# Optimization experiments

Hardware: AMD Instinct MI355X
Metric: run time of the kernel (lower is better)

The kernel has to match this reference:

```python
import jax, jax.numpy as jnp
import numpy as np

D_MODEL, D_FF, N_EXPERTS, TOP_K = 1024, 4096, 8, 2


def setup_inputs() -> dict:
    key = jax.random.key(0)
    ks = jax.random.split(key, 7)
    s = 0.02
    return {
        "x": jax.random.normal(ks[0], (2, 2048, D_MODEL), dtype=jnp.float32),
        "router_w": jax.random.normal(ks[1], (D_MODEL, N_EXPERTS), dtype=jnp.float32) * s,
        "router_b": jnp.zeros((N_EXPERTS,), dtype=jnp.float32),
        "w1": jax.random.normal(ks[2], (N_EXPERTS, D_MODEL, D_FF), dtype=jnp.float32) * s,
        "b1": jnp.zeros((N_EXPERTS, D_FF), dtype=jnp.float32),
        "w2": jax.random.normal(ks[3], (N_EXPERTS, D_FF, D_MODEL), dtype=jnp.float32) * s,
        "b2": jnp.zeros((N_EXPERTS, D_MODEL), dtype=jnp.float32),
    }


def reference(x, router_w, router_b, w1, b1, w2, b2):
    bsz, seq_len, d_model = x.shape
    flat_x = x.reshape(-1, d_model)                      # [T, D]
    logits = flat_x @ router_w + router_b                # [T, E]
    topk_scores, topk_idx = jax.lax.top_k(logits, TOP_K) # [T, K]
    gates = jax.nn.softmax(topk_scores, axis=-1).astype(flat_x.dtype)
    mixed = jnp.zeros_like(flat_x)
    num_experts = w1.shape[0]
    for e in range(num_experts):
        # dense per-expert MLP over all tokens; tokens not routed to e get weight 0,
        # so the math matches the original gather-MLP-scatter exactly.
        h = jax.nn.gelu(flat_x @ w1[e] + b1[e], approximate=False)  # exact GELU as torch nn.GELU
        y = h @ w2[e] + b2[e]                                       # [T, D]
        w_e = jnp.sum(jnp.where(topk_idx == e, gates, 0.0), axis=-1, keepdims=True)  # [T, 1]
        mixed = mixed + w_e * y
    return mixed.reshape(bsz, seq_len, d_model)
```

## Files before the change

### kernel.cpp

```cpp
#include <hip/hip_runtime.h>
#include <hip/hip_bf16.h>
#include <stdint.h>

#define T_TOK 4096
#define DM 1024
#define DF 4096
#define NE 8
#define PADROWS 10240

typedef __attribute__((ext_vector_type(8))) short short8;
typedef __attribute__((ext_vector_type(8))) unsigned short ushort8_t;
typedef __attribute__((ext_vector_type(4))) float f32x4;

__device__ __forceinline__ unsigned short f2bf(float f) {
    union { float f; unsigned u; } v; v.f = f;
    unsigned r = v.u + 0x7fffu + ((v.u >> 16) & 1u);
    return (unsigned short)(r >> 16);
}

__device__ __forceinline__ void async_cp16(const void* g, void* l) {
    __builtin_amdgcn_global_load_lds(
        (const __attribute__((address_space(1))) unsigned*)g,
        (__attribute__((address_space(3))) unsigned*)l,
        16, 0, 0);
}

#define WAITV(n)  asm volatile("s_waitcnt vmcnt(" #n ")" ::: "memory")
#define WAITLGKM() asm volatile("s_waitcnt lgkmcnt(0)" ::: "memory")
#define BAR()     asm volatile("s_barrier" ::: "memory")

__device__ __forceinline__ int swz(int g, int r) { return g ^ (r & 3) ^ ((r >> 2) & 3); }

__global__ __launch_bounds__(256) void k_router(
    const float* __restrict__ x, const float* __restrict__ rw,
    const float* __restrict__ rb, int* __restrict__ counts,
    int* __restrict__ listTok, int4* __restrict__ tokRec,
    float2* __restrict__ tokGate)
{
    int l  = threadIdx.x & 63;
    int wv = threadIdx.x >> 6;
    int t  = blockIdx.x * 4 + wv;
    const float* xr = x + (size_t)t * DM;
    float acc[NE];
#pragma unroll
    for (int e = 0; e < NE; ++e) acc[e] = 0.f;
#pragma unroll
    for (int i = 0; i < 16; ++i) {
        int d = i * 64 + l;
        float xv = xr[d];
        const float4* wp = (const float4*)(rw + (size_t)d * NE);
        float4 w0 = wp[0], w1 = wp[1];
        acc[0] += xv * w0.x; acc[1] += xv * w0.y; acc[2] += xv * w0.z; acc[3] += xv * w0.w;
        acc[4] += xv * w1.x; acc[5] += xv * w1.y; acc[6] += xv * w1.z; acc[7] += xv * w1.w;
    }
#pragma unroll
    for (int off = 32; off >= 1; off >>= 1)
#pragma unroll
        for (int e = 0; e < NE; ++e) acc[e] += __shfl_down(acc[e], off);
    if (l == 0) {
        float lg[NE];
#pragma unroll
        for (int e = 0; e < NE; ++e) lg[e] = acc[e] + rb[e];
        int i1 = 0; float s1 = lg[0];
#pragma unroll
        for (int e = 1; e < NE; ++e) if (lg[e] > s1) { s1 = lg[e]; i1 = e; }
        int i2 = -1; float s2 = -3.0e38f;
#pragma unroll
        for (int e = 0; e < NE; ++e) if (e != i1 && lg[e] > s2) { s2 = lg[e]; i2 = e; }
        float g1 = 1.f / (1.f + expf(s2 - s1));
        float g2 = 1.f - g1;
        int p1 = atomicAdd(&counts[i1], 1);
        listTok[i1 * T_TOK + p1] = t;
        int p2 = atomicAdd(&counts[i2], 1);
        listTok[i2 * T_TOK + p2] = t;
        tokRec[t]  = make_int4(i1, p1, i2, p2);
        tokGate[t] = make_float2(g1, g2);
    }
}

__global__ void k_offsets(const int* __restrict__ counts, int* __restrict__ offsets)
{
    int cum = 0;
    for (int e = 0; e < NE; ++e) { offsets[e] = cum; cum += (counts[e] + 255) & ~255; }
    offsets[NE] = cum;
}

__global__ __launch_bounds__(256) void k_packw(const float* __restrict__ src,
                                               unsigned short* __restrict__ dst,
                                               int K, int N)
{
    __shared__ float tile[64][65];
    int e  = blockIdx.z;
    int n0 = blockIdx.x * 64;
    int k0 = blockIdx.y * 64;
    const float* s    = src + (size_t)e * K * N;
    unsigned short* d = dst + (size_t)e * K * N;
    int tid = threadIdx.x;
#pragma unroll
    for (int i = 0; i < 4; ++i) {
        int u  = i * 256 + tid;
        int kk = u >> 4;
        int nn = (u & 15) * 4;
        float4 v = *(const float4*)(s + (size_t)(k0 + kk) * N + n0 + nn);
        tile[kk][nn] = v.x; tile[kk][nn + 1] = v.y; tile[kk][nn + 2] = v.z; tile[kk][nn + 3] = v.w;
    }
    __syncthreads();
#pragma unroll
    for (int i = 0; i < 2; ++i) {
        int u  = i * 256 + tid;
        int nn = u >> 3;
        int kg = u & 7;
        int gg = kg & 3;
        int n  = n0 + nn;
        ushort8_t o;
#pragma unroll
        for (int j = 0; j < 8; ++j) o[j] = f2bf(tile[kg * 8 + j][nn]);
        size_t slab = (size_t)(k0 >> 5) + (kg >> 2);
        *(ushort8_t*)(d + (slab * N + n) * 32 + (swz(gg, n) << 3)) = o;
    }
}

__global__ __launch_bounds__(256) void k_packa(
    const float* __restrict__ x, const int* __restrict__ listTok,
    const int* __restrict__ counts, const int* __restrict__ offsets,
    unsigned short* __restrict__ ap)
{
    int r0   = blockIdx.x * 64;
    int slab = blockIdx.y;
    int tid  = threadIdx.x;
    __shared__ int toks[64];
    if (tid < 64) {
        int r = r0 + tid;
        int tok = 0;
        int total = offsets[NE];
        if (r < total) {
            int e = 0;
#pragma unroll
            for (int j = 1; j < NE; ++j) if (r >= offsets[j]) e = j;
            int local = r - offsets[e];
            int c = counts[e];
            if (local >= c) local = c - 1;
            if (local < 0) local = 0;
            tok = (c > 0) ? listTok[e * T_TOK + local] : 0;
        }
        toks[tid] = tok;
    }
    __syncthreads();
    int rl = tid >> 2, gg = tid & 3;
    int tok = toks[rl];
    const float4* src = (const float4*)(x + (size_t)tok * DM + slab * 32 + gg * 8);
    float4 v0 = src[0], v1 = src[1];
    ushort8_t o;
    o[0] = f2bf(v0.x); o[1] = f2bf(v0.y); o[2] = f2bf(v0.z); o[3] = f2bf(v0.w);
    o[4] = f2bf(v1.x); o[5] = f2bf(v1.y); o[6] = f2bf(v1.z); o[7] = f2bf(v1.w);
    int rr = r0 + rl;
    *(ushort8_t*)(ap + ((size_t)slab * PADROWS + rr) * 32 + (swz(gg, rr) << 3)) = o;
}

__global__ __launch_bounds__(512, 2) void k_ffn1(
    const unsigned short* __restrict__ ap, const unsigned short* __restrict__ w1p,
    const float* __restrict__ b1, const int* __restrict__ counts,
    const int* __restrict__ offsets, unsigned short* __restrict__ Hp)
{
    __shared__ __align__(16) unsigned short lds[65536];
    int i = blockIdx.x;
    int L = (i & 7) * 256 + (i >> 3);
    int mt = L & 15, grp = L >> 4;
    int y = grp & 15, e = grp >> 4;
    int cnt = counts[e];
    int m0  = mt << 8;
    if (m0 >= cnt) return;
    int R0 = offsets[e] + m0;
    int n0 = y << 8;

    int tid = threadIdx.x, wv = tid >> 6, l = tid & 63;
    int wm = wv >> 2, wn = wv & 3;
    int g = l >> 4, lr = l & 15;

    int offA[8], offB[4];
#pragma unroll
    for (int mi = 0; mi < 8; ++mi) {
        int r = wm * 128 + mi * 16 + lr;
        offA[mi] = r * 32 + (swz(g, r) << 3);
    }
#pragma unroll
    for (int ni = 0; ni < 4; ++ni) {
        int r = wn * 64 + ni * 16 + lr;
        offB[ni] = 8192 + r * 32 + (swz(g, r) << 3);
    }

    const unsigned short* gA = ap + (size_t)R0 * 32;
    const unsigned short* gB = w1p + (size_t)e * DM * DF + (size_t)n0 * 32;

    f32x4 acc[8][4];
#pragma unroll
    for (int a = 0; a < 8; ++a)
#pragma unroll
        for (int b = 0; b < 4; ++b) acc[a][b] = (f32x4)(0.f);

#define STAGE1(t) { \
    unsigned short* sb = lds + (((t) & 3) << 14); \
    const unsigned short* ga = gA + (size_t)(t) * (PADROWS * 32); \
    const unsigned short* gb = gB + (size_t)(t) * (DF * 32); \
    int c0 = wv * 512; \
    async_cp16(ga + c0 + l * 8,        sb + c0); \
    async_cp16(ga + 4096 + c0 + l * 8, sb + 4096 + c0); \
    async_cp16(gb + c0 + l * 8,        sb + 8192 + c0); \
    async_cp16(gb + 4096 + c0 + l * 8, sb + 12288 + c0); }

#define COMPUTE1(t) { \
    const unsigned short* sb = lds + (((t) & 3) << 14); \
    short8 aF[8], bF[4]; \
    _Pragma("unroll") for (int ni = 0; ni < 4; ++ni) bF[ni] = *(const short8*)(sb + offB[ni]); \
    _Pragma("unroll") for (int mi = 0; mi < 8; ++mi) aF[mi] = *(const short8*)(sb + offA[mi]); \
    __builtin_amdgcn_s_setprio(1); \
    _Pragma("unroll") for (int mi = 0; mi < 8; ++mi) \
    _Pragma("unroll") for (int ni = 0; ni < 4; ++ni) \
        acc[mi][ni] = __builtin_amdgcn_mfma_f32_16x16x32_bf16(aF[mi], bF[ni], acc[mi][ni], 0, 0, 0); \
    __builtin_amdgcn_s_setprio(0); }

    STAGE1(0); STAGE1(1); STAGE1(2);
    for (int t = 0; t < 29; ++t) {
        STAGE1(t + 3);
        WAITV(12); BAR();
        COMPUTE1(t);
        BAR();
    }
    WAITV(8); BAR(); COMPUTE1(29); BAR();
    WAITV(4); BAR(); COMPUTE1(30); BAR();
    WAITV(0); BAR(); COMPUTE1(31); BAR();

#pragma unroll
    for (int ni = 0; ni < 4; ++ni) {
        int nloc = wn * 64 + ni * 16 + lr;
        float bias = b1[e * DF + n0 + nloc];
        int slab = nloc >> 5, c = nloc & 31, g2 = c >> 3;
#pragma unroll
        for (int mi = 0; mi < 8; ++mi) {
#pragma unroll
            for (int rg = 0; rg < 4; ++rg) {
                int m = wm * 128 + mi * 16 + g * 4 + rg;
                float v = acc[mi][ni][rg] + bias;
                v = 0.5f * v * (1.f + erff(v * 0.70710678118f));
                lds[(slab << 13) + m * 32 + (swz(g2, m) << 3) + (c & 7)] = f2bf(v);
            }
        }
    }
    WAITLGKM(); BAR();
#pragma unroll
    for (int j = 0; j < 16; ++j) {
        int u = j * 512 + tid;
        int elem = u * 8;
        int slab = elem >> 13;
        int rem  = elem & 8191;
        *(ushort8_t*)(Hp + ((size_t)((n0 >> 5) + slab) * PADROWS + R0) * 32 + rem) =
            *(const ushort8_t*)(lds + elem);
    }
}

__global__ __launch_bounds__(512, 2) void k_ffn2(
    const unsigned short* __restrict__ Hp, const unsigned short* __restrict__ w2p,
    const float* __restrict__ b2, const int* __restrict__ counts,
    const int* __restrict__ offsets, float* __restrict__ ypart)
{
    __shared__ __align__(16) unsigned short lds[49152];
    int i = blockIdx.x;
    int L = (i & 7) * 128 + (i >> 3);
    int mt = L & 15, grp = L >> 4;
    int y = grp & 7, e = grp >> 3;
    int cnt = counts[e];
    int m0  = mt << 8;
    if (m0 >= cnt) return;
    int R0 = offsets[e] + m0;
    int n0 = y << 7;

    int tid = threadIdx.x, wv = tid >> 6, l = tid & 63;
    int wm = wv >> 1, wn = wv & 1;
    int g = l >> 4, lr = l & 15;

    int offA[4], offB[4];
#pragma unroll
    for (int mi = 0; mi < 4; ++mi) {
        int r = wm * 64 + mi * 16 + lr;
        offA[mi] = r * 32 + (swz(g, r) << 3);
    }
#pragma unroll
    for (int ni = 0; ni < 4; ++ni) {
        int r = wn * 64 + ni * 16 + lr;
        offB[ni] = 8192 + r * 32 + (swz(g, r) << 3);
    }

    const unsigned short* gA = Hp + (size_t)R0 * 32;
    const unsigned short* gB = w2p + (size_t)e * DF * DM + (size_t)n0 * 32;

    f32x4 acc[4][4];
#pragma unroll
    for (int a = 0; a < 4; ++a)
#pragma unroll
        for (int b = 0; b < 4; ++b) acc[a][b] = (f32x4)(0.f);

#define STAGE2(t) { \
    unsigned short* sb = lds + ((t) & 3) * 12288; \
    const unsigned short* ga = gA + (size_t)(t) * (PADROWS * 32); \
    const unsigned short* gb = gB + (size_t)(t) * (DM * 32); \
    int c0 = wv * 512; \
    async_cp16(ga + c0 + l * 8,        sb + c0); \
    async_cp16(ga + 4096 + c0 + l * 8, sb + 4096 + c0); \
    async_cp16(gb + c0 + l * 8,        sb + 8192 + c0); }

#define COMPUTE2(t) { \
    const unsigned short* sb = lds + ((t) & 3) * 12288; \
    short8 aF[4], bF[4]; \
    _Pragma("unroll") for (int ni = 0; ni < 4; ++ni) bF[ni] = *(const short8*)(sb + offB[ni]); \
    _Pragma("unroll") for (int mi = 0; mi < 4; ++mi) aF[mi] = *(const short8*)(sb + offA[mi]); \
    __builtin_amdgcn_s_setprio(1); \
    _Pragma("unroll") for (int mi = 0; mi < 4; ++mi) \
    _Pragma("unroll") for (int ni = 0; ni < 4; ++ni) \
        acc[mi][ni] = __builtin_amdgcn_mfma_f32_16x16x32_bf16(aF[mi], bF[ni], acc[mi][ni], 0, 0, 0); \
    __builtin_amdgcn_s_setprio(0); }

    STAGE2(0); STAGE2(1); STAGE2(2);
    for (int t = 0; t < 125; ++t) {
        STAGE2(t + 3);
        WAITV(9); BAR();
        COMPUTE2(t);
        BAR();
    }
    WAITV(6); BAR(); COMPUTE2(125); BAR();
    WAITV(3); BAR(); COMPUTE2(126); BAR();
    WAITV(0); BAR(); COMPUTE2(127); BAR();

    float bias[4];
#pragma unroll
    for (int ni = 0; ni < 4; ++ni) bias[ni] = b2[e * DM + n0 + wn * 64 + ni * 16 + lr];
#pragma unroll
    for (int mi = 0; mi < 4; ++mi) {
#pragma unroll
        for (int rg = 0; rg < 4; ++rg) {
            int m = wm * 64 + mi * 16 + g * 4 + rg;
            size_t row = (size_t)R0 + m;
#pragma unroll
            for (int ni = 0; ni < 4; ++ni) {
                ypart[row * DM + n0 + wn * 64 + ni * 16 + lr] = acc[mi][ni][rg] + bias[ni];
            }
        }
    }
}

__global__ __launch_bounds__(256) void k_gather(
    const float* __restrict__ yp, const int4* __restrict__ rec,
    const float2* __restrict__ gg, const int* __restrict__ offsets,
    float* __restrict__ out)
{
    int t = blockIdx.x;
    int4 rc = rec[t];
    float2 w = gg[t];
    size_t r1 = (size_t)offsets[rc.x] + rc.y;
    size_t r2 = (size_t)offsets[rc.z] + rc.w;
    const float4* a = (const float4*)(yp + r1 * DM);
    const float4* b = (const float4*)(yp + r2 * DM);
    float4 va = a[threadIdx.x], vb = b[threadIdx.x];
    float4 o;
    o.x = w.x * va.x + w.y * vb.x;
    o.y = w.x * va.y + w.y * vb.y;
    o.z = w.x * va.z + w.y * vb.z;
    o.w = w.x * va.w + w.y * vb.w;
    ((float4*)(out + (size_t)t * DM))[threadIdx.x] = o;
}

extern "C" void kernel_launch(void* const* d_in, const int* in_sizes, int n_in,
                              void* d_out, int out_size, void* d_ws, size_t ws_size,
                              hipStream_t stream)
{
    const float* x  = (const float*)d_in[0];
    const float* rw = (const float*)d_in[1];
    const float* rb = (const float*)d_in[2];
    const float* w1 = (const float*)d_in[3];
    const float* b1 = (const float*)d_in[4];
    const float* w2 = (const float*)d_in[5];
    const float* b2 = (const float*)d_in[6];
    float* out = (float*)d_out;

    char* ws = (char*)d_ws;
    int*            counts   = (int*)(ws + 0);
    int*            offsets  = (int*)(ws + 128);
    int*            listTok  = (int*)(ws + 512);
    unsigned short* apack    = (unsigned short*)(ws + 262656);
    unsigned short* w2p      = (unsigned short*)(ws + 262656);
    unsigned short* w1p      = (unsigned short*)(ws + 21234176);
    unsigned short* Hp       = (unsigned short*)(ws + 88343040);
    float*          ypart    = (float*)(ws + 172229120);
    int4*           tokRec   = (int4*)(ws + 214172160);
    float2*         tokGate  = (float2*)(ws + 214237696);

    hipMemsetAsync(counts, 0, 32, stream);

    k_router <<<T_TOK / 4, 256, 0, stream>>>(x, rw, rb, counts, listTok, tokRec, tokGate);
    k_offsets<<<1, 1, 0, stream>>>(counts, offsets);
    k_packw  <<<dim3(DF / 64, DM / 64, NE), 256, 0, stream>>>(w1, w1p, DM, DF);
    k_packa  <<<dim3(PADROWS / 64, 32), 256, 0, stream>>>(x, listTok, counts, offsets, apack);
    k_ffn1   <<<2048, 512, 0, stream>>>(apack, w1p, b1, counts, offsets, Hp);
    k_packw  <<<dim3(DM / 64, DF / 64, NE), 256, 0, stream>>>(w2, w2p, DF, DM);
    k_ffn2   <<<1024, 512, 0, stream>>>(Hp, w2p, b2, counts, offsets, ypart);
    k_gather <<<T_TOK, 256, 0, stream>>>(ypart, tokRec, tokGate, offsets, out);
}
```

Before: 755.4 us.

## Widen K slabs to 64 and interleave half-tile loads with MFMA phases

Repacks weights, activations and the hidden buffer into 64-wide K slabs with an XOR-by-row swizzle instead of 32-wide slabs. Both FFN GEMM kernels switch from a 4-deep ring of small stages to double-buffered 64-K tiles. Each tile is split into four quarter-phases, and async loads for the next tiles are issued between MFMA groups. The aim is fewer barriers per K step and finer overlap of global-to-LDS copies with matrix math. The cost is more barriers inside each tile and a shallower prefetch depth, which may expose memory latency.

```diff
diff --git a/kernel.cpp b/kernel.cpp
--- a/kernel.cpp
+++ b/kernel.cpp
@@ -25,11 +25,9 @@
         16, 0, 0);
 }
 
-#define WAITV(n)  asm volatile("s_waitcnt vmcnt(" #n ")" ::: "memory")
+#define WAITV(n)   asm volatile("s_waitcnt vmcnt(" #n ")" ::: "memory")
 #define WAITLGKM() asm volatile("s_waitcnt lgkmcnt(0)" ::: "memory")
-#define BAR()     asm volatile("s_barrier" ::: "memory")
-
-__device__ __forceinline__ int swz(int g, int r) { return g ^ (r & 3) ^ ((r >> 2) & 3); }
+#define BAR()      asm volatile("s_barrier" ::: "memory")
 
 __global__ __launch_bounds__(256) void k_router(
     const float* __restrict__ x, const float* __restrict__ rw,
@@ -106,17 +104,19 @@
     }
     __syncthreads();
 #pragma unroll
-    for (int i = 0; i < 2; ++i) {
+    for (int i = 0; i < 4; ++i) {
         int u  = i * 256 + tid;
-        int nn = u >> 3;
-        int kg = u & 7;
-        int gg = kg & 3;
+        int nn = u >> 4;
+        int g  = (u >> 1) & 7;
+        int h  = (u & 1) * 4;
+        int kc = g * 8 + h;
         int n  = n0 + nn;
-        ushort8_t o;
-#pragma unroll
-        for (int j = 0; j < 8; ++j) o[j] = f2bf(tile[kg * 8 + j][nn]);
-        size_t slab = (size_t)(k0 >> 5) + (kg >> 2);
-        *(ushort8_t*)(d + (slab * N + n) * 32 + (swz(gg, n) << 3)) = o;
+        ushort4 o;
+        o.x = f2bf(tile[kc + 0][nn]); o.y = f2bf(tile[kc + 1][nn]);
+        o.z = f2bf(tile[kc + 2][nn]); o.w = f2bf(tile[kc + 3][nn]);
+        int gp = g ^ (n & 7);
+        size_t off = ((size_t)(k0 >> 6) * N + n) * 64 + gp * 8 + h;
+        *(ushort4*)(d + off) = o;
     }
 }
 
@@ -125,9 +125,9 @@
     const int* __restrict__ counts, const int* __restrict__ offsets,
     unsigned short* __restrict__ ap)
 {
-    int r0   = blockIdx.x * 64;
-    int slab = blockIdx.y;
-    int tid  = threadIdx.x;
+    int r0  = blockIdx.x * 64;
+    int kt  = blockIdx.y;
+    int tid = threadIdx.x;
     __shared__ int toks[64];
     if (tid < 64) {
         int r = r0 + tid;
@@ -146,15 +146,20 @@
         toks[tid] = tok;
     }
     __syncthreads();
-    int rl = tid >> 2, gg = tid & 3;
-    int tok = toks[rl];
-    const float4* src = (const float4*)(x + (size_t)tok * DM + slab * 32 + gg * 8);
-    float4 v0 = src[0], v1 = src[1];
-    ushort8_t o;
-    o[0] = f2bf(v0.x); o[1] = f2bf(v0.y); o[2] = f2bf(v0.z); o[3] = f2bf(v0.w);
-    o[4] = f2bf(v1.x); o[5] = f2bf(v1.y); o[6] = f2bf(v1.z); o[7] = f2bf(v1.w);
-    int rr = r0 + rl;
-    *(ushort8_t*)(ap + ((size_t)slab * PADROWS + rr) * 32 + (swz(gg, rr) << 3)) = o;
+#pragma unroll
+    for (int i = 0; i < 4; ++i) {
+        int u  = i * 256 + tid;
+        int rl = u >> 4;
+        int g  = (u >> 1) & 7;
+        int h  = (u & 1) * 4;
+        int tok = toks[rl];
+        float4 v = *(const float4*)(x + (size_t)tok * DM + kt * 64 + g * 8 + h);
+        ushort4 o; o.x = f2bf(v.x); o.y = f2bf(v.y); o.z = f2bf(v.z); o.w = f2bf(v.w);
+        int row = r0 + rl;
+        int gp  = g ^ (row & 7);
+        size_t off = ((size_t)kt * PADROWS + row) * 64 + gp * 8 + h;
+        *(ushort4*)(ap + off) = o;
+    }
 }
 
 __global__ __launch_bounds__(512, 2) void k_ffn1(
@@ -163,6 +168,7 @@
     const int* __restrict__ offsets, unsigned short* __restrict__ Hp)
 {
     __shared__ __align__(16) unsigned short lds[65536];
+    const int NT = 16;
     int i = blockIdx.x;
     int L = (i & 7) * 256 + (i >> 3);
     int mt = L & 15, grp = L >> 4;
@@ -175,22 +181,14 @@
 
     int tid = threadIdx.x, wv = tid >> 6, l = tid & 63;
     int wm = wv >> 2, wn = wv & 3;
-    int g = l >> 4, lr = l & 15;
-
-    int offA[8], offB[4];
-#pragma unroll
-    for (int mi = 0; mi < 8; ++mi) {
-        int r = wm * 128 + mi * 16 + lr;
-        offA[mi] = r * 32 + (swz(g, r) << 3);
-    }
-#pragma unroll
-    for (int ni = 0; ni < 4; ++ni) {
-        int r = wn * 64 + ni * 16 + lr;
-        offB[ni] = 8192 + r * 32 + (swz(g, r) << 3);
-    }
-
-    const unsigned short* gA = ap + (size_t)R0 * 32;
-    const unsigned short* gB = w1p + (size_t)e * DM * DF + (size_t)n0 * 32;
+    int g4 = l >> 4, lr = l & 15;
+    int gp0 = g4 ^ (lr & 7);
+    int dK  = ((gp0 ^ 4) - gp0) * 8;
+    int baseA = (wm * 128 + lr) * 64 + gp0 * 8;
+    int baseB = 16384 + (wn * 64 + lr) * 64 + gp0 * 8;
+
+    const unsigned short* gA = ap + (size_t)R0 * 64;
+    const unsigned short* gB = w1p + (size_t)e * DM * DF + (size_t)n0 * 64;
 
     f32x4 acc[8][4];
 #pragma unroll
@@ -198,51 +196,80 @@
 #pragma unroll
         for (int b = 0; b < 4; ++b) acc[a][b] = (f32x4)(0.f);
 
-#define STAGE1(t) { \
-    unsigned short* sb = lds + (((t) & 3) << 14); \
-    const unsigned short* ga = gA + (size_t)(t) * (PADROWS * 32); \
-    const unsigned short* gb = gB + (size_t)(t) * (DF * 32); \
-    int c0 = wv * 512; \
-    async_cp16(ga + c0 + l * 8,        sb + c0); \
-    async_cp16(ga + 4096 + c0 + l * 8, sb + 4096 + c0); \
-    async_cp16(gb + c0 + l * 8,        sb + 8192 + c0); \
-    async_cp16(gb + 4096 + c0 + l * 8, sb + 12288 + c0); }
-
-#define COMPUTE1(t) { \
-    const unsigned short* sb = lds + (((t) & 3) << 14); \
-    short8 aF[8], bF[4]; \
-    _Pragma("unroll") for (int ni = 0; ni < 4; ++ni) bF[ni] = *(const short8*)(sb + offB[ni]); \
-    _Pragma("unroll") for (int mi = 0; mi < 8; ++mi) aF[mi] = *(const short8*)(sb + offA[mi]); \
-    __builtin_amdgcn_s_setprio(1); \
-    _Pragma("unroll") for (int mi = 0; mi < 8; ++mi) \
-    _Pragma("unroll") for (int ni = 0; ni < 4; ++ni) \
-        acc[mi][ni] = __builtin_amdgcn_mfma_f32_16x16x32_bf16(aF[mi], bF[ni], acc[mi][ni], 0, 0, 0); \
-    __builtin_amdgcn_s_setprio(0); }
-
-    STAGE1(0); STAGE1(1); STAGE1(2);
-    for (int t = 0; t < 29; ++t) {
-        STAGE1(t + 3);
-        WAITV(12); BAR();
-        COMPUTE1(t);
-        BAR();
-    }
-    WAITV(8); BAR(); COMPUTE1(29); BAR();
-    WAITV(4); BAR(); COMPUTE1(30); BAR();
-    WAITV(0); BAR(); COMPUTE1(31); BAR();
+#define ST_A1(T, h) { int ch = wv * 2; \
+    const unsigned short* gp_ = gA + (size_t)(T) * (PADROWS * 64) + (h) * 8192; \
+    unsigned short* dp_ = lds + ((T) & 1) * 32768 + (h) * 8192; \
+    async_cp16(gp_ + ch * 512 + l * 8, dp_ + ch * 512); \
+    async_cp16(gp_ + (ch + 1) * 512 + l * 8, dp_ + (ch + 1) * 512); }
+
+#define ST_B1(T, h) { int ch = wv * 2; \
+    const unsigned short* gp_ = gB + (size_t)(T) * (DF * 64) + (h) * 8192; \
+    unsigned short* dp_ = lds + ((T) & 1) * 32768 + 16384 + (h) * 8192; \
+    async_cp16(gp_ + ch * 512 + l * 8, dp_ + ch * 512); \
+    async_cp16(gp_ + (ch + 1) * 512 + l * 8, dp_ + (ch + 1) * 512); }
+
+#define RD_A1(MH) { _Pragma("unroll") for (int mi = 0; mi < 4; ++mi) { \
+    aF[mi][0] = *(const short8*)(sb + baseA + ((MH) * 4 + mi) * 1024); \
+    aF[mi][1] = *(const short8*)(sb + baseA + ((MH) * 4 + mi) * 1024 + dK); } }
+
+#define RD_B1(DST, NH) { _Pragma("unroll") for (int ni = 0; ni < 2; ++ni) { \
+    DST[ni][0] = *(const short8*)(sb + baseB + ((NH) * 2 + ni) * 1024); \
+    DST[ni][1] = *(const short8*)(sb + baseB + ((NH) * 2 + ni) * 1024 + dK); } }
+
+#define MM16(MH, BF, NB) \
+    _Pragma("unroll") for (int ks = 0; ks < 2; ++ks) \
+    _Pragma("unroll") for (int mi = 0; mi < 4; ++mi) \
+    _Pragma("unroll") for (int ni = 0; ni < 2; ++ni) \
+        acc[(MH) * 4 + mi][(NB) + ni] = __builtin_amdgcn_mfma_f32_16x16x32_bf16( \
+            aF[mi][ks], BF[ni][ks], acc[(MH) * 4 + mi][(NB) + ni], 0, 0, 0);
+
+    ST_A1(0, 0); ST_A1(0, 1); ST_B1(0, 0); ST_B1(0, 1);
+    ST_B1(1, 0); ST_A1(1, 0);
+    WAITV(4); BAR();
+
+    for (int T = 0; T < NT; ++T) {
+        unsigned short* sb = lds + (T & 1) * 32768;
+        short8 aF[4][2], bH0[2][2], bF1[2][2];
+        RD_A1(0); RD_B1(bH0, 0);
+        if (T + 1 < NT) ST_A1(T + 1, 1);
+        BAR(); WAITLGKM();
+        __builtin_amdgcn_s_setprio(1); MM16(0, bH0, 0); __builtin_amdgcn_s_setprio(0);
+        BAR();
+        RD_B1(bF1, 1);
+        if (T + 1 < NT) ST_B1(T + 1, 1);
+        BAR(); WAITLGKM();
+        __builtin_amdgcn_s_setprio(1); MM16(0, bF1, 2); __builtin_amdgcn_s_setprio(0);
+        BAR();
+        RD_A1(1);
+        if (T + 2 < NT) ST_B1(T + 2, 0);
+        BAR(); WAITLGKM();
+        __builtin_amdgcn_s_setprio(1); MM16(1, bF1, 2); __builtin_amdgcn_s_setprio(0);
+        BAR();
+        if (T + 2 < NT) ST_A1(T + 2, 0);
+        if (T == NT - 2) { WAITV(0); } else if (T < NT - 2) { WAITV(4); }
+        BAR();
+        __builtin_amdgcn_s_setprio(1); MM16(1, bH0, 0); __builtin_amdgcn_s_setprio(0);
+        BAR();
+    }
+#undef ST_A1
+#undef ST_B1
+#undef RD_A1
+#undef RD_B1
+#undef MM16
 
 #pragma unroll
     for (int ni = 0; ni < 4; ++ni) {
         int nloc = wn * 64 + ni * 16 + lr;
         float bias = b1[e * DF + n0 + nloc];
-        int slab = nloc >> 5, c = nloc & 31, g2 = c >> 3;
+        int slab = nloc >> 6, kc = nloc & 63, gg = kc >> 3, kr = kc & 7;
 #pragma unroll
         for (int mi = 0; mi < 8; ++mi) {
 #pragma unroll
             for (int rg = 0; rg < 4; ++rg) {
-                int m = wm * 128 + mi * 16 + g * 4 + rg;
+                int m = wm * 128 + mi * 16 + g4 * 4 + rg;
                 float v = acc[mi][ni][rg] + bias;
                 v = 0.5f * v * (1.f + erff(v * 0.70710678118f));
-                lds[(slab << 13) + m * 32 + (swz(g2, m) << 3) + (c & 7)] = f2bf(v);
+                lds[slab * 16384 + m * 64 + ((gg ^ (m & 7)) << 3) + kr] = f2bf(v);
             }
         }
     }
@@ -251,9 +278,9 @@
     for (int j = 0; j < 16; ++j) {
         int u = j * 512 + tid;
         int elem = u * 8;
-        int slab = elem >> 13;
-        int rem  = elem & 8191;
-        *(ushort8_t*)(Hp + ((size_t)((n0 >> 5) + slab) * PADROWS + R0) * 32 + rem) =
+        int slab = elem >> 14;
+        int rem  = elem & 16383;
+        *(ushort8_t*)(Hp + ((size_t)((n0 >> 6) + slab) * PADROWS + R0) * 64 + rem) =
             *(const ushort8_t*)(lds + elem);
     }
 }
@@ -264,6 +291,7 @@
     const int* __restrict__ offsets, float* __restrict__ ypart)
 {
     __shared__ __align__(16) unsigned short lds[49152];
+    const int NT = 64;
     int i = blockIdx.x;
     int L = (i & 7) * 128 + (i >> 3);
     int mt = L & 15, grp = L >> 4;
@@ -276,73 +304,93 @@
 
     int tid = threadIdx.x, wv = tid >> 6, l = tid & 63;
     int wm = wv >> 1, wn = wv & 1;
-    int g = l >> 4, lr = l & 15;
-
-    int offA[4], offB[4];
+    int g4 = l >> 4, lr = l & 15;
+    int gp0 = g4 ^ (lr & 7);
+    int dK  = ((gp0 ^ 4) - gp0) * 8;
+    int baseA = (wm * 64 + lr) * 64 + gp0 * 8;
+    int baseB = 16384 + (wn * 64 + lr) * 64 + gp0 * 8;
+
+    const unsigned short* gA = Hp + (size_t)R0 * 64;
+    const unsigned short* gB = w2p + (size_t)e * DF * DM + (size_t)n0 * 64;
+
+    f32x4 acc[4][4];
+#pragma unroll
+    for (int a = 0; a < 4; ++a)
+#pragma unroll
+        for (int b = 0; b < 4; ++b) acc[a][b] = (f32x4)(0.f);
+
+#define ST_A2(T, h) { int ch = wv * 2; \
+    const unsigned short* gp_ = gA + (size_t)(T) * (PADROWS * 64) + (h) * 8192; \
+    unsigned short* dp_ = lds + ((T) & 1) * 24576 + (h) * 8192; \
+    async_cp16(gp_ + ch * 512 + l * 8, dp_ + ch * 512); \
+    async_cp16(gp_ + (ch + 1) * 512 + l * 8, dp_ + (ch + 1) * 512); }
+
+#define ST_B2(T, h) { \
+    const unsigned short* gp_ = gB + (size_t)(T) * (DM * 64) + (h) * 4096; \
+    unsigned short* dp_ = lds + ((T) & 1) * 24576 + 16384 + (h) * 4096; \
+    async_cp16(gp_ + wv * 512 + l * 8, dp_ + wv * 512); }
+
+#define RD_A2(MH) { _Pragma("unroll") for (int mi = 0; mi < 2; ++mi) { \
+    aF[mi][0] = *(const short8*)(sb + baseA + ((MH) * 2 + mi) * 1024); \
+    aF[mi][1] = *(const short8*)(sb + baseA + ((MH) * 2 + mi) * 1024 + dK); } }
+
+#define RD_B2(DST, NH) { _Pragma("unroll") for (int ni = 0; ni < 2; ++ni) { \
+    DST[ni][0] = *(const short8*)(sb + baseB + ((NH) * 2 + ni) * 1024); \
+    DST[ni][1] = *(const short8*)(sb + baseB + ((NH) * 2 + ni) * 1024 + dK); } }
+
+#define MM8(MH, BF, NB) \
+    _Pragma("unroll") for (int ks = 0; ks < 2; ++ks) \
+    _Pragma("unroll") for (int mi = 0; mi < 2; ++mi) \
+    _Pragma("unroll") for (int ni = 0; ni < 2; ++ni) \
+        acc[(MH) * 2 + mi][(NB) + ni] = __builtin_amdgcn_mfma_f32_16x16x32_bf16( \
+            aF[mi][ks], BF[ni][ks], acc[(MH) * 2 + mi][(NB) + ni], 0, 0, 0);
+
+    ST_A2(0, 0); ST_A2(0, 1); ST_B2(0, 0); ST_B2(0, 1);
+    ST_B2(1, 0); ST_A2(1, 0);
+    WAITV(3); BAR();
+
+    for (int T = 0; T < NT; ++T) {
+        unsigned short* sb = lds + (T & 1) * 24576;
+        short8 aF[2][2], bH0[2][2], bF1[2][2];
+        RD_A2(0); RD_B2(bH0, 0);
+        if (T + 1 < NT) ST_A2(T + 1, 1);
+        BAR(); WAITLGKM();
+        __builtin_amdgcn_s_setprio(1); MM8(0, bH0, 0); __builtin_amdgcn_s_setprio(0);
+        BAR();
+        RD_B2(bF1, 1);
+        if (T + 1 < NT) ST_B2(T + 1, 1);
+        BAR(); WAITLGKM();
+        __builtin_amdgcn_s_setprio(1); MM8(0, bF1, 2); __builtin_amdgcn_s_setprio(0);
+        BAR();
+        RD_A2(1);
+        if (T + 2 < NT) ST_B2(T + 2, 0);
+        BAR(); WAITLGKM();
+        __builtin_amdgcn_s_setprio(1); MM8(1, bF1, 2); __builtin_amdgcn_s_setprio(0);
+        BAR();
+        if (T + 2 < NT) ST_A2(T + 2, 0);
+        if (T == NT - 2) { WAITV(0); } else if (T < NT - 2) { WAITV(3); }
+        BAR();
+        __builtin_amdgcn_s_setprio(1); MM8(1, bH0, 0); __builtin_amdgcn_s_setprio(0);
+        BAR();
+    }
+#undef ST_A2
+#undef ST_B2
+#undef RD_A2
+#undef RD_B2
+#undef MM8
+
+    float bias[4];
+#pragma unroll
+    for (int ni = 0; ni < 4; ++ni) bias[ni] = b2[e * DM + n0 + wn * 64 + ni * 16 + lr];
 #pragma unroll
     for (int mi = 0; mi < 4; ++mi) {
-        int r = wm * 64 + mi * 16 + lr;
-        offA[mi] = r * 32 + (swz(g, r) << 3);
-    }
-#pragma unroll
-    for (int ni = 0; ni < 4; ++ni) {
-        int r = wn * 64 + ni * 16 + lr;
-        offB[ni] = 8192 + r * 32 + (swz(g, r) << 3);
-    }
-
-    const unsigned short* gA = Hp + (size_t)R0 * 32;
-    const unsigned short* gB = w2p + (size_t)e * DF * DM + (size_t)n0 * 32;
-
-    f32x4 acc[4][4];
-#pragma unroll
-    for (int a = 0; a < 4; ++a)
-#pragma unroll
-        for (int b = 0; b < 4; ++b) acc[a][b] = (f32x4)(0.f);
-
-#define STAGE2(t) { \
-    unsigned short* sb = lds + ((t) & 3) * 12288; \
-    const unsigned short* ga = gA + (size_t)(t) * (PADROWS * 32); \
-    const unsigned short* gb = gB + (size_t)(t) * (DM * 32); \
-    int c0 = wv * 512; \
-    async_cp16(ga + c0 + l * 8,        sb + c0); \
-    async_cp16(ga + 4096 + c0 + l * 8, sb + 4096 + c0); \
-    async_cp16(gb + c0 + l * 8,        sb + 8192 + c0); }
-
-#define COMPUTE2(t) { \
-    const unsigned short* sb = lds + ((t) & 3) * 12288; \
-    short8 aF[4], bF[4]; \
-    _Pragma("unroll") for (int ni = 0; ni < 4; ++ni) bF[ni] = *(const short8*)(sb + offB[ni]); \
-    _Pragma("unroll") for (int mi = 0; mi < 4; ++mi) aF[mi] = *(const short8*)(sb + offA[mi]); \
-    __builtin_amdgcn_s_setprio(1); \
-    _Pragma("unroll") for (int mi = 0; mi < 4; ++mi) \
-    _Pragma("unroll") for (int ni = 0; ni < 4; ++ni) \
-        acc[mi][ni] = __builtin_amdgcn_mfma_f32_16x16x32_bf16(aF[mi], bF[ni], acc[mi][ni], 0, 0, 0); \
-    __builtin_amdgcn_s_setprio(0); }
-
-    STAGE2(0); STAGE2(1); STAGE2(2);
-    for (int t = 0; t < 125; ++t) {
-        STAGE2(t + 3);
-        WAITV(9); BAR();
-        COMPUTE2(t);
-        BAR();
-    }
-    WAITV(6); BAR(); COMPUTE2(125); BAR();
-    WAITV(3); BAR(); COMPUTE2(126); BAR();
-    WAITV(0); BAR(); COMPUTE2(127); BAR();
-
-    float bias[4];
-#pragma unroll
-    for (int ni = 0; ni < 4; ++ni) bias[ni] = b2[e * DM + n0 + wn * 64 + ni * 16 + lr];
-#pragma unroll
-    for (int mi = 0; mi < 4; ++mi) {
 #pragma unroll
         for (int rg = 0; rg < 4; ++rg) {
-            int m = wm * 64 + mi * 16 + g * 4 + rg;
-            size_t row = (size_t)R0 + m;
-#pragma unroll
-            for (int ni = 0; ni < 4; ++ni) {
-                ypart[row * DM + n0 + wn * 64 + ni * 16 + lr] = acc[mi][ni][rg] + bias[ni];
-            }
+            int m = wm * 64 + mi * 16 + g4 * 4 + rg;
+            float* orow = ypart + ((size_t)R0 + m) * DM;
+#pragma unroll
+            for (int ni = 0; ni < 4; ++ni)
+                orow[n0 + wn * 64 + ni * 16 + lr] = acc[mi][ni][rg] + bias[ni];
         }
     }
 }
@@ -398,7 +446,7 @@
     k_router <<<T_TOK / 4, 256, 0, stream>>>(x, rw, rb, counts, listTok, tokRec, tokGate);
     k_offsets<<<1, 1, 0, stream>>>(counts, offsets);
     k_packw  <<<dim3(DF / 64, DM / 64, NE), 256, 0, stream>>>(w1, w1p, DM, DF);
-    k_packa  <<<dim3(PADROWS / 64, 32), 256, 0, stream>>>(x, listTok, counts, offsets, apack);
+    k_packa  <<<dim3(PADROWS / 64, 16), 256, 0, stream>>>(x, listTok, counts, offsets, apack);
     k_ffn1   <<<2048, 512, 0, stream>>>(apack, w1p, b1, counts, offsets, Hp);
     k_packw  <<<dim3(DM / 64, DF / 64, NE), 256, 0, stream>>>(w2, w2p, DF, DM);
     k_ffn2   <<<1024, 512, 0, stream>>>(Hp, w2p, b2, counts, offsets, ypart);
```

After: 724.3 us. 4.1% less time.
